# Kernel optimization log

Measured on AMD Instinct MI355X. Metric: run time of the kernel, lower is better.

The kernel has to match this reference:

```python
import jax, jax.numpy as jnp
import numpy as np
import math

B, S, D = 4, 1024, 1024
E, DE = 8, 128            # n_experts, expert_dim (D == E*DE)
TOPK = 2
SCALE = 1.0 / math.sqrt(D)  # source divides by sqrt(self.dim) = sqrt(transformer_dim)


def setup_inputs() -> dict:
    key = jax.random.key(0)
    k1, k2, k3, k4, k5 = jax.random.split(key, 5)
    Q = jax.random.normal(k1, (B, S, D), dtype=jnp.float32)
    K = jax.random.normal(k2, (B, S, D), dtype=jnp.float32)
    V = jax.random.normal(k3, (B, S, D), dtype=jnp.float32)
    route_prob = jax.random.uniform(k4, (B, E), dtype=jnp.float32)
    # first-stage MoE dispatch (idx_list): expert_mask[e, b] == 1 iff batch b routed to expert e
    expert_mask = jax.random.randint(k5, (E, B), 0, 2).astype(jnp.int32)
    mask = jnp.ones((B, S), dtype=jnp.float32)  # accepted but unused by the source forward
    return {"Q": Q, "K": K, "V": V, "route_prob": route_prob,
            "expert_mask": expert_mask, "mask": mask}


def reference(Q, K, V, route_prob, expert_mask, mask):
    # RowParallelMatmulWithMoE: each expert e attends using its 128-wide feature slice
    Qe = Q.reshape(B, S, E, DE)
    Ke = K.reshape(B, S, E, DE)
    scores = jnp.einsum('bsed,bted->ebst', Qe, Ke) * SCALE   # [E, B, S, S]
    probs = jax.nn.softmax(scores, axis=-1)                   # per-expert softmax (dropout p=0)
    # index_add_ scatter: sum routed experts' attention maps per batch element
    m1 = expert_mask.astype(Q.dtype)                          # [E, B]
    attn = jnp.einsum('eb,ebst->bst', m1, probs)              # [B, S, S]
    # preprocess: top-k expert re-selection from route_prob -> new idx_list
    _, top_idx = jax.lax.top_k(route_prob, TOPK)              # [B, TOPK]
    m2 = jnp.zeros((B, E), dtype=Q.dtype).at[jnp.arange(B)[:, None], top_idx].set(1.0)
    # ColumnParallelMatmulWithMoE: attn @ V restricted to each selected expert's V slice
    Ve = V.reshape(B, S, E, DE)
    out = jnp.einsum('bst,bted->bsed', attn, Ve) * m2[:, None, :, None]  # [B, S, E, DE]
    return out.reshape(B, S, D)
```

## Files before the change

### kernel.cpp

```cpp
#include <hip/hip_runtime.h>
#include <hip/hip_bf16.h>
#include <stdint.h>

#define B_ 4
#define S_ 1024
#define E_ 8
#define DE_ 128
#define SCALE_ 0.03125f

typedef __attribute__((ext_vector_type(8))) short short8;
typedef __attribute__((ext_vector_type(4))) float f32x4;
typedef unsigned short ushort_t;
typedef unsigned int uint32;

__device__ __forceinline__ ushort_t f2bf(float f) {
    uint32 u = __float_as_uint(f);
    uint32 r = u + 0x7fffu + ((u >> 16) & 1u);
    return (ushort_t)(r >> 16);
}

#define GLOAD_LDS16(g, l) __builtin_amdgcn_global_load_lds( \
    (const __attribute__((address_space(1))) unsigned int*)(g), \
    (__attribute__((address_space(3))) unsigned int*)(l), 16, 0, 0)

__device__ __forceinline__ void stage16(const ushort_t* __restrict__ g,
                                        size_t stride, ushort_t* lds,
                                        int w, int lane) {
    int cb = w << 6;
    int ch = cb + lane;
    int r = ch >> 4, c = ch & 15;
    GLOAD_LDS16(g + (size_t)r * stride + ((c ^ (r & 7)) << 3),
                lds + ((size_t)cb << 3));
}
__device__ __forceinline__ void stage128(const ushort_t* __restrict__ g,
                                         size_t stride, ushort_t* lds,
                                         int w, int lane) {
    #pragma unroll
    for (int j = 0; j < 8; ++j) {
        int cb = (w * 8 + j) << 6;
        int ch = cb + lane;
        int r = ch >> 4, c = ch & 15;
        GLOAD_LDS16(g + (size_t)r * stride + ((c ^ (r & 7)) << 3),
                    lds + ((size_t)cb << 3));
    }
}
__device__ __forceinline__ short8 fld(const ushort_t* lds, int row, int c) {
    return *(const short8*)(lds + (((row << 4) + (c ^ (row & 7))) << 3));
}

__device__ __forceinline__ void top2(const float* rp, int& i1, int& i2) {
    float v1 = rp[0]; i1 = 0;
    #pragma unroll
    for (int i = 1; i < 8; ++i) { float v = rp[i]; if (v > v1) { v1 = v; i1 = i; } }
    float v2 = -1e30f; i2 = 0;
    #pragma unroll
    for (int i = 0; i < 8; ++i) {
        if (i == i1) continue;
        float v = rp[i]; if (v > v2) { v2 = v; i2 = i; }
    }
}

__global__ __launch_bounds__(256) void prep_kernel(
        const float* __restrict__ Q, const float* __restrict__ K,
        const float* __restrict__ V, const float* __restrict__ route,
        const int* __restrict__ em,
        ushort_t* __restrict__ Qb, ushort_t* __restrict__ Kb,
        ushort_t* __restrict__ Vt, float* __restrict__ out) {
    __shared__ ushort_t tile[64][130];
    const int tid = threadIdx.x;
    const int sc = blockIdx.x, e = blockIdx.y, b = blockIdx.z;
    const int s0 = sc * 64;
    const size_t plane = ((size_t)(b * 8 + e)) << 17;

    const bool ak = em[e * B_ + b] != 0;
    int i1, i2; top2(route + b * 8, i1, i2);
    const bool av = (e == i1) || (e == i2);

    if (!av) {
        #pragma unroll
        for (int i = 0; i < 8; ++i) {
            int idx = tid + i * 256, r = idx >> 5, c4 = idx & 31;
            *(float4*)(out + (((size_t)(b * 1024 + s0 + r)) << 10) + (e << 7) + (c4 << 2))
                = make_float4(0.f, 0.f, 0.f, 0.f);
        }
    }
    if (ak) {
        #pragma unroll
        for (int i = 0; i < 8; ++i) {
            int idx = tid + i * 256, r = idx >> 5, c4 = idx & 31;
            size_t in_off = ((size_t)(b * 1024 + s0 + r) << 10) + (e << 7) + (c4 << 2);
            float4 q = *(const float4*)(Q + in_off);
            float4 k = *(const float4*)(K + in_off);
            size_t oo = plane + (((size_t)(s0 + r)) << 7) + (c4 << 2);
            *(ushort4*)(Qb + oo) = make_ushort4(f2bf(q.x), f2bf(q.y), f2bf(q.z), f2bf(q.w));
            *(ushort4*)(Kb + oo) = make_ushort4(f2bf(k.x), f2bf(k.y), f2bf(k.z), f2bf(k.w));
        }
    }
    if (av) {
        #pragma unroll
        for (int i = 0; i < 8; ++i) {
            int idx = tid + i * 256, r = idx >> 5, c4 = idx & 31;
            size_t in_off = ((size_t)(b * 1024 + s0 + r) << 10) + (e << 7) + (c4 << 2);
            float4 v = *(const float4*)(V + in_off);
            ushort_t* p = &tile[r][c4 << 2];
            p[0] = f2bf(v.x); p[1] = f2bf(v.y); p[2] = f2bf(v.z); p[3] = f2bf(v.w);
        }
        __syncthreads();
        #pragma unroll
        for (int i = 0; i < 4; ++i) {
            int item = tid + i * 256, d = item & 127, sg = item >> 7;
            union { uint4 q; ushort_t u[8]; } tmp;
            #pragma unroll
            for (int j = 0; j < 8; ++j) tmp.u[j] = tile[sg * 8 + j][d];
            *(uint4*)(Vt + plane + (((size_t)d) << 10) + s0 + (sg << 3)) = tmp.q;
        }
    }
}

__global__ __launch_bounds__(256, 1) void attn_mega(
        const ushort_t* __restrict__ Qb, const ushort_t* __restrict__ Kb,
        const ushort_t* __restrict__ Vt, const float* __restrict__ route,
        const int* __restrict__ em, float* __restrict__ out) {

    __shared__ __align__(16) ushort_t kt[2][128 * 128];
    __shared__ __align__(16) ushort_t qt[2][16 * 128];
    __shared__ __align__(16) ushort_t attnL[16 * 1024];
    __shared__ float red[4][16];

    const int stile = blockIdx.x, b = blockIdx.y;
    const int s0 = stile * 16;
    const int tid = threadIdx.x;
    const int w = tid >> 6, lane = tid & 63;
    const int quad = lane >> 4, l16 = lane & 15;

    uint32 epack = 0; int ne = 0;
    #pragma unroll
    for (int e = 0; e < 8; ++e)
        if (em[e * B_ + b] != 0) { epack |= (uint32)e << (3 * ne); ++ne; }
    int i1, i2; top2(route + b * 8, i1, i2);

    f32x4 aacc[8][2];
    #pragma unroll
    for (int c = 0; c < 8; ++c)
        #pragma unroll
        for (int n = 0; n < 2; ++n) aacc[c][n] = (f32x4){0.f, 0.f, 0.f, 0.f};

    if (ne > 0) {
        {
            int e0 = epack & 7;
            size_t pl = ((size_t)(b * 8 + e0)) << 17;
            stage16(Qb + pl + ((size_t)s0 << 7), 128, qt[0], w, lane);
            stage128(Kb + pl, 128, kt[0], w, lane);
        }
        __syncthreads();

        for (int i = 0; i < ne; ++i) {
            int e = (epack >> (3 * i)) & 7;
            size_t pl = ((size_t)(b * 8 + e)) << 17;

            short8 af[4];
            #pragma unroll
            for (int kk = 0; kk < 4; ++kk)
                af[kk] = fld(qt[i & 1], l16, kk * 4 + quad);

            float rsum[4] = {0.f, 0.f, 0.f, 0.f};
            f32x4 pstr[8][2];

            #pragma unroll
            for (int c = 0; c < 8; ++c) {
                int g = i * 8 + c;
                if (c < 7) {
                    stage128(Kb + pl + (((size_t)(c + 1)) << 14), 128,
                             kt[(g + 1) & 1], w, lane);
                } else if (i + 1 < ne) {
                    int en = (epack >> (3 * (i + 1))) & 7;
                    size_t pln = ((size_t)(b * 8 + en)) << 17;
                    stage16(Qb + pln + ((size_t)s0 << 7), 128, qt[(i + 1) & 1], w, lane);
                    stage128(Kb + pln, 128, kt[(g + 1) & 1], w, lane);
                }
                const ushort_t* kb = kt[g & 1];
                f32x4 sacc[2];
                sacc[0] = (f32x4){0.f, 0.f, 0.f, 0.f};
                sacc[1] = (f32x4){0.f, 0.f, 0.f, 0.f};
                #pragma unroll
                for (int n = 0; n < 2; ++n)
                    #pragma unroll
                    for (int kk = 0; kk < 4; ++kk) {
                        short8 bf = fld(kb, w * 32 + n * 16 + l16, kk * 4 + quad);
                        sacc[n] = __builtin_amdgcn_mfma_f32_16x16x32_bf16(
                            af[kk], bf, sacc[n], 0, 0, 0);
                    }
                #pragma unroll
                for (int n = 0; n < 2; ++n)
                    #pragma unroll
                    for (int r = 0; r < 4; ++r) {
                        float p = __expf(sacc[n][r] * SCALE_);
                        pstr[c][n][r] = p;
                        rsum[r] += p;
                    }
                __syncthreads();
            }

            #pragma unroll
            for (int off = 1; off < 16; off <<= 1)
                #pragma unroll
                for (int r = 0; r < 4; ++r)
                    rsum[r] += __shfl_xor(rsum[r], off, 64);
            if (l16 == 0) {
                #pragma unroll
                for (int r = 0; r < 4; ++r) red[w][quad * 4 + r] = rsum[r];
            }
            __syncthreads();
            float rinv[4];
            #pragma unroll
            for (int r = 0; r < 4; ++r)
                rinv[r] = 1.0f / (red[0][quad * 4 + r] + red[1][quad * 4 + r] +
                                  red[2][quad * 4 + r] + red[3][quad * 4 + r]);
            #pragma unroll
            for (int c = 0; c < 8; ++c)
                #pragma unroll
                for (int n = 0; n < 2; ++n)
                    #pragma unroll
                    for (int r = 0; r < 4; ++r)
                        aacc[c][n][r] += pstr[c][n][r] * rinv[r];
        }
    }

    #pragma unroll
    for (int c = 0; c < 8; ++c)
        #pragma unroll
        for (int n = 0; n < 2; ++n)
            #pragma unroll
            for (int r = 0; r < 4; ++r) {
                int row = quad * 4 + r;
                int t = c * 128 + w * 32 + n * 16 + l16;
                int ct = t >> 3, lo = t & 7;
                attnL[(row << 10) + (((ct ^ (row & 7)) << 3) | lo)] =
                    f2bf(aacc[c][n][r]);
            }
    stage128(Vt + (((size_t)(b * 8 + i1)) << 17), 1024, kt[0], w, lane);
    __syncthreads();

    int selE[2] = {i1, i2};
    f32x4 oacc[2][2];
    #pragma unroll
    for (int s = 0; s < 2; ++s)
        #pragma unroll
        for (int n = 0; n < 2; ++n) oacc[s][n] = (f32x4){0.f, 0.f, 0.f, 0.f};

    for (int sel = 0; sel < 2; ++sel) {
        size_t vpl = ((size_t)(b * 8 + selE[sel])) << 17;
        #pragma unroll
        for (int c = 0; c < 8; ++c) {
            int g = sel * 8 + c;
            if (c < 7)
                stage128(Vt + vpl + ((c + 1) * 128), 1024, kt[(g + 1) & 1], w, lane);
            else if (sel == 0)
                stage128(Vt + (((size_t)(b * 8 + selE[1])) << 17), 1024,
                         kt[(g + 1) & 1], w, lane);
            const ushort_t* vb = kt[g & 1];
            short8 af2[4];
            #pragma unroll
            for (int kk = 0; kk < 4; ++kk) {
                int ct = c * 16 + kk * 4 + quad;
                af2[kk] = *(const short8*)&attnL[(l16 << 10) + (((ct ^ (l16 & 7)) << 3))];
            }
            #pragma unroll
            for (int n = 0; n < 2; ++n)
                #pragma unroll
                for (int kk = 0; kk < 4; ++kk) {
                    short8 bf = fld(vb, w * 32 + n * 16 + l16, kk * 4 + quad);
                    oacc[sel][n] = __builtin_amdgcn_mfma_f32_16x16x32_bf16(
                        af2[kk], bf, oacc[sel][n], 0, 0, 0);
                }
            __syncthreads();
        }
    }

    #pragma unroll
    for (int sel = 0; sel < 2; ++sel)
        #pragma unroll
        for (int n = 0; n < 2; ++n)
            #pragma unroll
            for (int r = 0; r < 4; ++r)
                out[(((size_t)(b * 1024 + s0 + quad * 4 + r)) << 10)
                    + selE[sel] * 128 + w * 32 + n * 16 + l16] = oacc[sel][n][r];
}

extern "C" void kernel_launch(void* const* d_in, const int* in_sizes, int n_in,
                              void* d_out, int out_size, void* d_ws, size_t ws_size,
                              hipStream_t stream) {
    const float* Q     = (const float*)d_in[0];
    const float* K     = (const float*)d_in[1];
    const float* V     = (const float*)d_in[2];
    const float* route = (const float*)d_in[3];
    const int*   em    = (const int*)d_in[4];
    float* out = (float*)d_out;

    const size_t NB = (size_t)B_ * E_ * S_ * DE_;
    ushort_t* Qb = (ushort_t*)d_ws;
    ushort_t* Kb = Qb + NB;
    ushort_t* Vt = Kb + NB;

    dim3 gp(16, 8, 4);
    prep_kernel<<<gp, 256, 0, stream>>>(Q, K, V, route, em, Qb, Kb, Vt, out);
    dim3 gm(64, 4);
    attn_mega<<<gm, 256, 0, stream>>>(Qb, Kb, Vt, route, em, out);
}
```

Baseline: 150.3 us.

## Quantize Q/K to FP8 for QK^T MFMA and widen attention block to 512 threads

```diff
diff --git a/kernel.cpp b/kernel.cpp
--- a/kernel.cpp
+++ b/kernel.cpp
@@ -12,6 +12,8 @@
 typedef __attribute__((ext_vector_type(4))) float f32x4;
 typedef unsigned short ushort_t;
 typedef unsigned int uint32;
+typedef unsigned long long u64;
+typedef unsigned char uchar;
 
 __device__ __forceinline__ ushort_t f2bf(float f) {
     uint32 u = __float_as_uint(f);
@@ -19,33 +21,65 @@
     return (ushort_t)(r >> 16);
 }
 
+__device__ __forceinline__ uchar f2fp8(float f) {
+    float a = fminf(fmaxf(f, -448.f), 448.f);
+    uint32 u = __float_as_uint(a);
+    uint32 s = (u >> 31) << 7;
+    int ex = (int)((u >> 23) & 0xff);
+    uint32 man = u & 0x7fffff;
+    int e8 = ex - 127 + 7;
+    if (e8 >= 1) {
+        uint32 m = man >> 20;
+        uint32 rem = man & 0xfffff;
+        if (rem > 0x80000u || (rem == 0x80000u && (m & 1))) ++m;
+        if (m == 8) { m = 0; ++e8; }
+        if (e8 > 15) { e8 = 15; m = 6; }
+        return (uchar)(s | ((uint32)e8 << 3) | m);
+    } else {
+        int m = (int)rintf(fabsf(a) * 512.f);
+        if (m > 7) m = 7;
+        return (uchar)(s | (uint32)m);
+    }
+}
+
 #define GLOAD_LDS16(g, l) __builtin_amdgcn_global_load_lds( \
     (const __attribute__((address_space(1))) unsigned int*)(g), \
     (__attribute__((address_space(3))) unsigned int*)(l), 16, 0, 0)
 
-__device__ __forceinline__ void stage16(const ushort_t* __restrict__ g,
-                                        size_t stride, ushort_t* lds,
-                                        int w, int lane) {
-    int cb = w << 6;
-    int ch = cb + lane;
-    int r = ch >> 4, c = ch & 15;
-    GLOAD_LDS16(g + (size_t)r * stride + ((c ^ (r & 7)) << 3),
-                lds + ((size_t)cb << 3));
-}
-__device__ __forceinline__ void stage128(const ushort_t* __restrict__ g,
-                                         size_t stride, ushort_t* lds,
-                                         int w, int lane) {
-    #pragma unroll
-    for (int j = 0; j < 8; ++j) {
-        int cb = (w * 8 + j) << 6;
-        int ch = cb + lane;
-        int r = ch >> 4, c = ch & 15;
-        GLOAD_LDS16(g + (size_t)r * stride + ((c ^ (r & 7)) << 3),
-                    lds + ((size_t)cb << 3));
-    }
-}
-__device__ __forceinline__ short8 fld(const ushort_t* lds, int row, int c) {
-    return *(const short8*)(lds + (((row << 4) + (c ^ (row & 7))) << 3));
+__device__ __forceinline__ void stageK32(const uchar* g, uchar* lds, int tid) {
+    #pragma unroll
+    for (int k2 = 0; k2 < 4; ++k2) {
+        int u = tid + k2 * 512;
+        int r = u >> 3, c = u & 7;
+        int cc = c ^ (r & 7);
+        GLOAD_LDS16(g + r * 128 + (cc << 4), lds + (u << 4));
+    }
+}
+__device__ __forceinline__ void stageV32(const uchar* g, uchar* lds, int tid) {
+    #pragma unroll
+    for (int k2 = 0; k2 < 4; ++k2) {
+        int u = tid + k2 * 512;
+        int r = u >> 4, c = u & 15;
+        int cc = (c & 8) | ((c & 7) ^ (r & 7));
+        GLOAD_LDS16(g + (size_t)r * 2048 + (cc << 4), lds + (u << 4));
+    }
+}
+__device__ __forceinline__ void stageQ(const uchar* g, uchar* lds, int tid) {
+    if (tid < 128) {
+        int r = tid >> 3, c = tid & 7;
+        int cc = c ^ (r & 7);
+        GLOAD_LDS16(g + r * 128 + (cc << 4), lds + (tid << 4));
+    }
+}
+__device__ __forceinline__ u64 fld8(const uchar* lds, int row, int kk, int quad) {
+    int c = kk * 2 + (quad >> 1);
+    int phys = c ^ (row & 7);
+    return *(const u64*)(lds + row * 128 + (phys << 4) + ((quad & 1) << 3));
+}
+__device__ __forceinline__ short8 fldv(const uchar* lds, int row, int kk, int quad) {
+    int c = kk * 4 + quad;
+    int phys = (c & 8) | ((c & 7) ^ (row & 7));
+    return *(const short8*)(lds + (size_t)row * 256 + (phys << 4));
 }
 
 __device__ __forceinline__ void top2(const float* rp, int& i1, int& i2) {
@@ -64,13 +98,13 @@
         const float* __restrict__ Q, const float* __restrict__ K,
         const float* __restrict__ V, const float* __restrict__ route,
         const int* __restrict__ em,
-        ushort_t* __restrict__ Qb, ushort_t* __restrict__ Kb,
+        uchar* __restrict__ Qb, uchar* __restrict__ Kb,
         ushort_t* __restrict__ Vt, float* __restrict__ out) {
     __shared__ ushort_t tile[64][130];
     const int tid = threadIdx.x;
     const int sc = blockIdx.x, e = blockIdx.y, b = blockIdx.z;
     const int s0 = sc * 64;
-    const size_t plane = ((size_t)(b * 8 + e)) << 17;
+    const size_t plane8 = ((size_t)(b * 8 + e)) << 17;
 
     const bool ak = em[e * B_ + b] != 0;
     int i1, i2; top2(route + b * 8, i1, i2);
@@ -86,14 +120,24 @@
     }
     if (ak) {
         #pragma unroll
-        for (int i = 0; i < 8; ++i) {
-            int idx = tid + i * 256, r = idx >> 5, c4 = idx & 31;
-            size_t in_off = ((size_t)(b * 1024 + s0 + r) << 10) + (e << 7) + (c4 << 2);
-            float4 q = *(const float4*)(Q + in_off);
-            float4 k = *(const float4*)(K + in_off);
-            size_t oo = plane + (((size_t)(s0 + r)) << 7) + (c4 << 2);
-            *(ushort4*)(Qb + oo) = make_ushort4(f2bf(q.x), f2bf(q.y), f2bf(q.z), f2bf(q.w));
-            *(ushort4*)(Kb + oo) = make_ushort4(f2bf(k.x), f2bf(k.y), f2bf(k.z), f2bf(k.w));
+        for (int i = 0; i < 2; ++i) {
+            int u = tid + i * 256;
+            int r = u >> 3, dg = u & 7;
+            const float* qs = Q + ((size_t)(b * 1024 + s0 + r) << 10) + (e << 7) + (dg << 4);
+            const float* ks = K + ((size_t)(b * 1024 + s0 + r) << 10) + (e << 7) + (dg << 4);
+            union { uint4 w; uchar c[16]; } oq, ok;
+            #pragma unroll
+            for (int j = 0; j < 4; ++j) {
+                float4 qv = ((const float4*)qs)[j];
+                float4 kv = ((const float4*)ks)[j];
+                oq.c[j*4+0] = f2fp8(qv.x); oq.c[j*4+1] = f2fp8(qv.y);
+                oq.c[j*4+2] = f2fp8(qv.z); oq.c[j*4+3] = f2fp8(qv.w);
+                ok.c[j*4+0] = f2fp8(kv.x); ok.c[j*4+1] = f2fp8(kv.y);
+                ok.c[j*4+2] = f2fp8(kv.z); ok.c[j*4+3] = f2fp8(kv.w);
+            }
+            size_t oo = plane8 + ((size_t)(s0 + r) << 7) + (dg << 4);
+            *(uint4*)(Qb + oo) = oq.w;
+            *(uint4*)(Kb + oo) = ok.w;
         }
     }
     if (av) {
@@ -112,20 +156,21 @@
             union { uint4 q; ushort_t u[8]; } tmp;
             #pragma unroll
             for (int j = 0; j < 8; ++j) tmp.u[j] = tile[sg * 8 + j][d];
-            *(uint4*)(Vt + plane + (((size_t)d) << 10) + s0 + (sg << 3)) = tmp.q;
-        }
-    }
-}
-
-__global__ __launch_bounds__(256, 1) void attn_mega(
-        const ushort_t* __restrict__ Qb, const ushort_t* __restrict__ Kb,
+            *(uint4*)(Vt + (((size_t)(b * 8 + e)) << 17) + (((size_t)d) << 10)
+                      + s0 + (sg << 3)) = tmp.q;
+        }
+    }
+}
+
+__global__ __launch_bounds__(512, 1) void attn_mega(
+        const uchar* __restrict__ Qb, const uchar* __restrict__ Kb,
         const ushort_t* __restrict__ Vt, const float* __restrict__ route,
         const int* __restrict__ em, float* __restrict__ out) {
 
-    __shared__ __align__(16) ushort_t kt[2][128 * 128];
-    __shared__ __align__(16) ushort_t qt[2][16 * 128];
-    __shared__ __align__(16) ushort_t attnL[16 * 1024];
-    __shared__ float red[4][16];
+    __shared__ __align__(16) uchar kt[2][32768];
+    __shared__ __align__(16) uchar qt[2][2048];
+    __shared__ __align__(16) uchar attnL[32768];
+    __shared__ float red[8][16];
 
     const int stile = blockIdx.x, b = blockIdx.y;
     const int s0 = stile * 16;
@@ -139,73 +184,68 @@
         if (em[e * B_ + b] != 0) { epack |= (uint32)e << (3 * ne); ++ne; }
     int i1, i2; top2(route + b * 8, i1, i2);
 
-    f32x4 aacc[8][2];
-    #pragma unroll
-    for (int c = 0; c < 8; ++c)
+    f32x4 aacc[4][2];
+    #pragma unroll
+    for (int c = 0; c < 4; ++c)
         #pragma unroll
         for (int n = 0; n < 2; ++n) aacc[c][n] = (f32x4){0.f, 0.f, 0.f, 0.f};
 
     if (ne > 0) {
-        {
-            int e0 = epack & 7;
-            size_t pl = ((size_t)(b * 8 + e0)) << 17;
-            stage16(Qb + pl + ((size_t)s0 << 7), 128, qt[0], w, lane);
-            stage128(Kb + pl, 128, kt[0], w, lane);
-        }
+        int e0 = epack & 7;
+        stageQ(Qb + (((size_t)(b * 8 + e0)) << 17) + ((size_t)s0 << 7), qt[0], tid);
+        stageK32(Kb + (((size_t)(b * 8 + e0)) << 17), kt[0], tid);
         __syncthreads();
 
         for (int i = 0; i < ne; ++i) {
             int e = (epack >> (3 * i)) & 7;
-            size_t pl = ((size_t)(b * 8 + e)) << 17;
-
-            short8 af[4];
-            #pragma unroll
-            for (int kk = 0; kk < 4; ++kk)
-                af[kk] = fld(qt[i & 1], l16, kk * 4 + quad);
+            const uchar* kp = Kb + (((size_t)(b * 8 + e)) << 17);
+
+            u64 af[4];
+            #pragma unroll
+            for (int kk = 0; kk < 4; ++kk) af[kk] = fld8(qt[i & 1], l16, kk, quad);
 
             float rsum[4] = {0.f, 0.f, 0.f, 0.f};
-            f32x4 pstr[8][2];
-
-            #pragma unroll
-            for (int c = 0; c < 8; ++c) {
-                int g = i * 8 + c;
-                if (c < 7) {
-                    stage128(Kb + pl + (((size_t)(c + 1)) << 14), 128,
-                             kt[(g + 1) & 1], w, lane);
+            f32x4 ps[4][2];
+
+            #pragma unroll
+            for (int c = 0; c < 4; ++c) {
+                int g = i * 4 + c;
+                if (c < 3) {
+                    stageK32(kp + (size_t)(c + 1) * 32768, kt[(g + 1) & 1], tid);
                 } else if (i + 1 < ne) {
                     int en = (epack >> (3 * (i + 1))) & 7;
-                    size_t pln = ((size_t)(b * 8 + en)) << 17;
-                    stage16(Qb + pln + ((size_t)s0 << 7), 128, qt[(i + 1) & 1], w, lane);
-                    stage128(Kb + pln, 128, kt[(g + 1) & 1], w, lane);
+                    stageQ(Qb + (((size_t)(b * 8 + en)) << 17) + ((size_t)s0 << 7),
+                           qt[(i + 1) & 1], tid);
+                    stageK32(Kb + (((size_t)(b * 8 + en)) << 17), kt[(g + 1) & 1], tid);
+                } else {
+                    stageV32((const uchar*)(Vt + (((size_t)(b * 8 + i1)) << 17)),
+                             kt[(g + 1) & 1], tid);
                 }
-                const ushort_t* kb = kt[g & 1];
-                f32x4 sacc[2];
-                sacc[0] = (f32x4){0.f, 0.f, 0.f, 0.f};
-                sacc[1] = (f32x4){0.f, 0.f, 0.f, 0.f};
-                #pragma unroll
-                for (int n = 0; n < 2; ++n)
+                const uchar* kb = kt[g & 1];
+                #pragma unroll
+                for (int n = 0; n < 2; ++n) {
+                    f32x4 s = {0.f, 0.f, 0.f, 0.f};
+                    int trow = w * 32 + n * 16 + l16;
                     #pragma unroll
                     for (int kk = 0; kk < 4; ++kk) {
-                        short8 bf = fld(kb, w * 32 + n * 16 + l16, kk * 4 + quad);
-                        sacc[n] = __builtin_amdgcn_mfma_f32_16x16x32_bf16(
-                            af[kk], bf, sacc[n], 0, 0, 0);
+                        u64 bf = fld8(kb, trow, kk, quad);
+                        s = __builtin_amdgcn_mfma_f32_16x16x32_fp8_fp8(
+                            (long)af[kk], (long)bf, s, 0, 0, 0);
                     }
-                #pragma unroll
-                for (int n = 0; n < 2; ++n)
                     #pragma unroll
                     for (int r = 0; r < 4; ++r) {
-                        float p = __expf(sacc[n][r] * SCALE_);
-                        pstr[c][n][r] = p;
+                        float p = __expf(s[r] * SCALE_);
+                        ps[c][n][r] = p;
                         rsum[r] += p;
                     }
+                }
                 __syncthreads();
             }
 
             #pragma unroll
             for (int off = 1; off < 16; off <<= 1)
                 #pragma unroll
-                for (int r = 0; r < 4; ++r)
-                    rsum[r] += __shfl_xor(rsum[r], off, 64);
+                for (int r = 0; r < 4; ++r) rsum[r] += __shfl_xor(rsum[r], off, 64);
             if (l16 == 0) {
                 #pragma unroll
                 for (int r = 0; r < 4; ++r) red[w][quad * 4 + r] = rsum[r];
@@ -213,78 +253,68 @@
             __syncthreads();
             float rinv[4];
             #pragma unroll
-            for (int r = 0; r < 4; ++r)
-                rinv[r] = 1.0f / (red[0][quad * 4 + r] + red[1][quad * 4 + r] +
-                                  red[2][quad * 4 + r] + red[3][quad * 4 + r]);
-            #pragma unroll
-            for (int c = 0; c < 8; ++c)
+            for (int r = 0; r < 4; ++r) {
+                float l = 0.f;
+                #pragma unroll
+                for (int ww = 0; ww < 8; ++ww) l += red[ww][quad * 4 + r];
+                rinv[r] = 1.0f / l;
+            }
+            #pragma unroll
+            for (int c = 0; c < 4; ++c)
                 #pragma unroll
                 for (int n = 0; n < 2; ++n)
                     #pragma unroll
                     for (int r = 0; r < 4; ++r)
-                        aacc[c][n][r] += pstr[c][n][r] * rinv[r];
-        }
-    }
-
-    #pragma unroll
-    for (int c = 0; c < 8; ++c)
+                        aacc[c][n][r] += ps[c][n][r] * rinv[r];
+        }
+    } else {
+        stageV32((const uchar*)(Vt + (((size_t)(b * 8 + i1)) << 17)), kt[0], tid);
+    }
+
+    #pragma unroll
+    for (int c = 0; c < 4; ++c)
         #pragma unroll
         for (int n = 0; n < 2; ++n)
             #pragma unroll
             for (int r = 0; r < 4; ++r) {
                 int row = quad * 4 + r;
-                int t = c * 128 + w * 32 + n * 16 + l16;
-                int ct = t >> 3, lo = t & 7;
-                attnL[(row << 10) + (((ct ^ (row & 7)) << 3) | lo)] =
+                int t = c * 256 + w * 32 + n * 16 + l16;
+                int ct = t >> 3;
+                int phys = (ct & ~7) | ((ct & 7) ^ (row & 7));
+                *(ushort_t*)(attnL + row * 2048 + (phys << 4) + ((t & 7) << 1)) =
                     f2bf(aacc[c][n][r]);
             }
-    stage128(Vt + (((size_t)(b * 8 + i1)) << 17), 1024, kt[0], w, lane);
     __syncthreads();
 
     int selE[2] = {i1, i2};
-    f32x4 oacc[2][2];
-    #pragma unroll
-    for (int s = 0; s < 2; ++s)
-        #pragma unroll
-        for (int n = 0; n < 2; ++n) oacc[s][n] = (f32x4){0.f, 0.f, 0.f, 0.f};
-
+    #pragma unroll
     for (int sel = 0; sel < 2; ++sel) {
-        size_t vpl = ((size_t)(b * 8 + selE[sel])) << 17;
+        const uchar* vp = (const uchar*)(Vt + (((size_t)(b * 8 + selE[sel])) << 17));
+        f32x4 oacc = {0.f, 0.f, 0.f, 0.f};
         #pragma unroll
         for (int c = 0; c < 8; ++c) {
-            int g = sel * 8 + c;
+            int g = ne * 4 + sel * 8 + c;
             if (c < 7)
-                stage128(Vt + vpl + ((c + 1) * 128), 1024, kt[(g + 1) & 1], w, lane);
+                stageV32(vp + (size_t)(c + 1) * 256, kt[(g + 1) & 1], tid);
             else if (sel == 0)
-                stage128(Vt + (((size_t)(b * 8 + selE[1])) << 17), 1024,
-                         kt[(g + 1) & 1], w, lane);
-            const ushort_t* vb = kt[g & 1];
-            short8 af2[4];
+                stageV32((const uchar*)(Vt + (((size_t)(b * 8 + selE[1])) << 17)),
+                         kt[(g + 1) & 1], tid);
+            const uchar* vb = kt[g & 1];
             #pragma unroll
             for (int kk = 0; kk < 4; ++kk) {
                 int ct = c * 16 + kk * 4 + quad;
-                af2[kk] = *(const short8*)&attnL[(l16 << 10) + (((ct ^ (l16 & 7)) << 3))];
-            }
-            #pragma unroll
-            for (int n = 0; n < 2; ++n)
-                #pragma unroll
-                for (int kk = 0; kk < 4; ++kk) {
-                    short8 bf = fld(vb, w * 32 + n * 16 + l16, kk * 4 + quad);
-                    oacc[sel][n] = __builtin_amdgcn_mfma_f32_16x16x32_bf16(
-                        af2[kk], bf, oacc[sel][n], 0, 0, 0);
-                }
+                int phys = (ct & ~7) | ((ct & 7) ^ (l16 & 7));
+                short8 afr = *(const short8*)(attnL + l16 * 2048 + (phys << 4));
+                short8 bfr = fldv(vb, w * 16 + l16, kk, quad);
+                oacc = __builtin_amdgcn_mfma_f32_16x16x32_bf16(afr, bfr, oacc, 0, 0, 0);
+            }
             __syncthreads();
         }
-    }
-
-    #pragma unroll
-    for (int sel = 0; sel < 2; ++sel)
-        #pragma unroll
-        for (int n = 0; n < 2; ++n)
-            #pragma unroll
-            for (int r = 0; r < 4; ++r)
-                out[(((size_t)(b * 1024 + s0 + quad * 4 + r)) << 10)
-                    + selE[sel] * 128 + w * 32 + n * 16 + l16] = oacc[sel][n][r];
+        #pragma unroll
+        for (int r = 0; r < 4; ++r)
+            out[(((size_t)(b * 1024 + s0 + quad * 4 + r)) << 10)
+                + selE[sel] * 128 + w * 16 + l16] = oacc[r];
+    }
 }
 
 extern "C" void kernel_launch(void* const* d_in, const int* in_sizes, int n_in,
@@ -298,12 +328,12 @@
     float* out = (float*)d_out;
 
     const size_t NB = (size_t)B_ * E_ * S_ * DE_;
-    ushort_t* Qb = (ushort_t*)d_ws;
-    ushort_t* Kb = Qb + NB;
-    ushort_t* Vt = Kb + NB;
+    uchar* Qb = (uchar*)d_ws;
+    uchar* Kb = Qb + NB;
+    ushort_t* Vt = (ushort_t*)(Kb + NB);
 
     dim3 gp(16, 8, 4);
     prep_kernel<<<gp, 256, 0, stream>>>(Q, K, V, route, em, Qb, Kb, Vt, out);
     dim3 gm(64, 4);
-    attn_mega<<<gm, 256, 0, stream>>>(Qb, Kb, Vt, route, em, out);
-}
+    attn_mega<<<gm, 512, 0, stream>>>(Qb, Kb, Vt, route, em, out);
+}
```

Measured after the change: 135.5 us. -9.9%, faster.
